# Kernel tuning notes

Hardware: AMD Instinct MI355X
Metric: run time of the kernel (lower is better)

The kernel has to match this reference:

```python
import jax, jax.numpy as jnp
import numpy as np

B, NPG, IN_DIM, H, E = 128, 500, 3, 128, 512000
N = B * NPG
NEG = -1e9  # stands in for -inf masked fill; exp underflows to exactly 0 in fp32
BN_EPS = 1e-5


def setup_inputs() -> dict:
    key = jax.random.key(0)
    ks = jax.random.split(key, 40)
    rn = lambda k, shape: (jax.random.normal(k, shape, jnp.float32) * 0.05)
    x = jax.random.normal(ks[0], (N, IN_DIM), jnp.float32)
    g = jax.random.randint(ks[1], (E,), 0, B)
    src = jax.random.randint(ks[2], (E,), 0, NPG) + g * NPG
    dst = jax.random.randint(ks[3], (E,), 0, NPG) + g * NPG
    edge_index = jnp.stack([src, dst]).astype(jnp.int32)
    batch = (jnp.arange(N) // NPG).astype(jnp.int32)
    feasible_mask = jax.random.uniform(ks[4], (B, NPG, NPG)) < 0.1
    feasible_mask = feasible_mask.at[:, 0, 0].set(True)  # >=1 feasible action/graph
    return dict(
        x=x, edge_index=edge_index, batch=batch, feasible_mask=feasible_mask,
        gin_W1_0=rn(ks[5], (IN_DIM, H)), gin_b1_0=jnp.zeros((H,), jnp.float32),
        gin_g_0=jnp.ones((H,), jnp.float32), gin_be_0=jnp.zeros((H,), jnp.float32),
        gin_W2_0=rn(ks[6], (H, H)), gin_b2_0=jnp.zeros((H,), jnp.float32),
        gin_W1=rn(ks[7], (3, H, H)), gin_b1=jnp.zeros((3, H), jnp.float32),
        gin_g=jnp.ones((3, H), jnp.float32), gin_be=jnp.zeros((3, H), jnp.float32),
        gin_W2=rn(ks[8], (3, H, H)), gin_b2=jnp.zeros((3, H), jnp.float32),
        pol_W1_0=rn(ks[9], (2 * H, H)), pol_b1_0=jnp.zeros((H,), jnp.float32),
        pol_W2_0=rn(ks[10], (H, H)), pol_b2_0=jnp.zeros((H,), jnp.float32),
        pol_W1=rn(ks[11], (2, H, H)), pol_b1=jnp.zeros((2, H), jnp.float32),
        pol_W2=rn(ks[12], (2, H, H)), pol_b2=jnp.zeros((2, H), jnp.float32),
    )


def _gin_conv(h, src, dst, deg, W1, b1, g, be, W2, b2):
    # mean-aggregate neighbors (self loops already in edge list), eps=0
    agg = jax.ops.segment_sum(h[src], dst, num_segments=N) / deg[:, None]
    z = (h + agg) @ W1 + b1
    mu = jnp.mean(z, axis=0)
    var = jnp.var(z, axis=0)  # biased var, as torch BN training mode
    z = (z - mu) * jax.lax.rsqrt(var + BN_EPS) * g + be
    return jax.nn.relu(z) @ W2 + b2


def reference(x, edge_index, batch, feasible_mask,
              gin_W1_0, gin_b1_0, gin_g_0, gin_be_0, gin_W2_0, gin_b2_0,
              gin_W1, gin_b1, gin_g, gin_be, gin_W2, gin_b2,
              pol_W1_0, pol_b1_0, pol_W2_0, pol_b2_0,
              pol_W1, pol_b1, pol_W2, pol_b2):
    # add self loops
    loop = jnp.arange(N, dtype=edge_index.dtype)
    src = jnp.concatenate([edge_index[0], loop])
    dst = jnp.concatenate([edge_index[1], loop])
    deg = jnp.maximum(jax.ops.segment_sum(jnp.ones_like(src, jnp.float32), dst, num_segments=N), 1.0)

    h = _gin_conv(x, src, dst, deg, gin_W1_0, gin_b1_0, gin_g_0, gin_be_0, gin_W2_0, gin_b2_0)
    node_pool = h
    graph_pool = jax.ops.segment_sum(h, batch, num_segments=B) / NPG
    for l in range(3):
        h = _gin_conv(h, src, dst, deg, gin_W1[l], gin_b1[l], gin_g[l], gin_be[l], gin_W2[l], gin_b2[l])
        node_pool = node_pool + h
        graph_pool = graph_pool + jax.ops.segment_sum(h, batch, num_segments=B) / NPG

    # augment node embeds with their graph embed (graphs contiguous, equal size)
    a = jnp.concatenate([node_pool, graph_pool[batch]], axis=-1).reshape(B, NPG, 2 * H)
    a = jnp.tanh(a @ pol_W1_0 + pol_b1_0) @ pol_W2_0 + pol_b2_0
    for l in range(2):
        a = jnp.tanh(a @ pol_W1[l] + pol_b1[l]) @ pol_W2[l] + pol_b2[l]

    scores = jnp.einsum('bnd,bmd->bnm', a, a)                 # [B, n, n]
    scores = jnp.where(feasible_mask, scores, NEG)
    flat = scores.reshape(B, NPG * NPG)
    logp_all = jax.nn.log_softmax(flat, axis=-1)
    actions_id = jax.random.categorical(jax.random.key(42), flat, axis=-1)  # [B]
    log_prob = jnp.take_along_axis(logp_all, actions_id[:, None], axis=1)[:, 0]
    return actions_id, log_prob
```

## Files before the change

### kernel.cpp

```cpp
#include <hip/hip_runtime.h>
#include <float.h>

#define NN 64000
#define BB 128
#define NPGc 500
#define EE 512000

#define SKW(c) ((c) + (((c)>>3)<<2))
#define LW 188

__device__ __forceinline__ unsigned rotl32(unsigned x, unsigned r){ return (x<<r)|(x>>(32u-r)); }

__device__ __forceinline__ unsigned threefry_bits(unsigned idx){
  unsigned x0 = 0u, x1 = idx;
  const unsigned ks0 = 0u, ks1 = 42u, ks2 = 0u ^ 42u ^ 0x1BD11BDAu;
  x0 += ks0; x1 += ks1;
#define RND(r) { x0 += x1; x1 = rotl32(x1, r); x1 ^= x0; }
  RND(13u) RND(15u) RND(26u) RND(6u)   x0 += ks1; x1 += ks2 + 1u;
  RND(17u) RND(29u) RND(16u) RND(24u)  x0 += ks2; x1 += ks0 + 2u;
  RND(13u) RND(15u) RND(26u) RND(6u)   x0 += ks0; x1 += ks1 + 3u;
  RND(17u) RND(29u) RND(16u) RND(24u)  x0 += ks1; x1 += ks2 + 4u;
  RND(13u) RND(15u) RND(26u) RND(6u)   x0 += ks2; x1 += ks0 + 5u;
#undef RND
  return x0 ^ x1;
}

__device__ __forceinline__ float gumbel_of(unsigned idx){
  unsigned bits = threefry_bits(idx);
  float f = __uint_as_float((bits >> 9) | 0x3f800000u) - 1.0f;
  const float TINY = 1.17549435e-38f;
  float u = fmaxf(TINY, f + TINY);
  return -logf(-logf(u));
}

__device__ __forceinline__ float fast_tanh(float x){
  return 1.0f - 2.0f/(__expf(2.0f*x) + 1.0f);
}

__global__ __launch_bounds__(256)
void maskprep_kernel(const unsigned char* __restrict__ mu8src, const int* __restrict__ mi32src,
                     unsigned char* __restrict__ mn8, unsigned char* __restrict__ mt8){
  __shared__ unsigned char tile[64][65];
  const int b = blockIdx.y;
  const int rt = blockIdx.x >> 3, ct = blockIdx.x & 7;
  const int t = threadIdx.x;
  int mybad = (((const unsigned*)mi32src)[t] > 1u) ? 1 : 0;
  int isbool = __syncthreads_or(mybad);
  const int rl = t >> 4;
  const int cq = t & 15;
#pragma unroll
  for (int p=0;p<4;p++){
    int row = rt*64 + p*16 + rl;
    int col = ct*64 + cq*4;
    uchar4 v; v.x=0; v.y=0; v.z=0; v.w=0;
    if (row < NPGc && col < NPGc){
      size_t o = (size_t)b*250000 + (size_t)row*500 + col;
      if (isbool){
        v = *(const uchar4*)(mu8src + o);
      } else {
        int4 w = *(const int4*)(mi32src + o);
        v.x = (unsigned char)(w.x!=0); v.y = (unsigned char)(w.y!=0);
        v.z = (unsigned char)(w.z!=0); v.w = (unsigned char)(w.w!=0);
      }
      *(uchar4*)(mn8 + o) = v;
    }
    int lr = p*16 + rl, lc = cq*4;
    tile[lr][lc+0]=v.x; tile[lr][lc+1]=v.y; tile[lr][lc+2]=v.z; tile[lr][lc+3]=v.w;
  }
  __syncthreads();
#pragma unroll
  for (int p=0;p<4;p++){
    int orow = ct*64 + p*16 + rl;
    int ocol = rt*64 + cq*4;
    if (orow < NPGc && ocol < NPGc){
      uchar4 v;
      v.x = tile[cq*4+0][p*16+rl];
      v.y = tile[cq*4+1][p*16+rl];
      v.z = tile[cq*4+2][p*16+rl];
      v.w = tile[cq*4+3][p*16+rl];
      *(uchar4*)(mt8 + (size_t)b*250000 + (size_t)orow*500 + ocol) = v;
    }
  }
}

__global__ void count_kernel(const int* __restrict__ dst, int* __restrict__ cnt){
  int e = blockIdx.x*256 + threadIdx.x;
  if (e < EE) atomicAdd(&cnt[dst[e]], 1);
}

__global__ void scanA_kernel(const int* __restrict__ cnt, int* __restrict__ bsum){
  __shared__ int red[256];
  int t = threadIdx.x;
  red[t] = cnt[blockIdx.x*256 + t];
  __syncthreads();
  for (int s=128;s>0;s>>=1){
    if (t < s) red[t] += red[t+s];
    __syncthreads();
  }
  if (t == 0) bsum[blockIdx.x] = red[0];
}

__global__ void scanB_kernel(const int* __restrict__ bsum, int* __restrict__ boff){
  __shared__ int red[256];
  int t = threadIdx.x;
  int v = (t < 250) ? bsum[t] : 0;
  red[t] = v;
  __syncthreads();
  for (int d=1; d<256; d<<=1){
    int x = (t >= d) ? red[t-d] : 0;
    __syncthreads();
    red[t] += x;
    __syncthreads();
  }
  if (t < 250) boff[t] = red[t] - v;
  if (t == 249) boff[250] = red[t];
}

__global__ void scanC_kernel(const int* __restrict__ cnt, const int* __restrict__ boff,
                             int* __restrict__ off, int* __restrict__ cur){
  __shared__ int red[256];
  int t = threadIdx.x;
  int n = blockIdx.x*256 + t;
  int v = cnt[n];
  red[t] = v;
  __syncthreads();
  for (int d=1; d<256; d<<=1){
    int x = (t >= d) ? red[t-d] : 0;
    __syncthreads();
    red[t] += x;
    __syncthreads();
  }
  int excl = red[t] - v + boff[blockIdx.x];
  off[n] = excl; cur[n] = excl;
  if (n == NN-1) off[NN] = excl + v;
}

__global__ void fill_kernel(const int* __restrict__ src, const int* __restrict__ dst,
                            int* __restrict__ cur, int* __restrict__ csr){
  int e = blockIdx.x*256 + threadIdx.x;
  if (e < EE){
    int d = dst[e];
    int p = atomicAdd(&cur[d], 1);
    csr[p] = src[e];
  }
}

__global__ __launch_bounds__(256)
void agg128_kernel(const float* __restrict__ h, const int* __restrict__ off,
                   const int* __restrict__ csr, const int* __restrict__ cnt,
                   float* __restrict__ xin){
  const int nb = gridDim.x;
  const int per = nb >> 3;
  int bid = (blockIdx.x % 8)*per + (blockIdx.x >> 3);
  int w = (bid*256 + (int)threadIdx.x) >> 6;
  int lane = threadIdx.x & 63;
  if (w >= NN) return;
  const float* hn = h + (size_t)w*128;
  float a0 = hn[lane], a1 = hn[lane+64];
  float s0 = a0, s1 = a1;
  int e0 = off[w], e1 = off[w+1];
  int e = e0;
  for (; e + 4 <= e1; e += 4){
    int sA = csr[e], sB = csr[e+1], sC = csr[e+2], sD = csr[e+3];
    const float* pA = h + (size_t)sA*128;
    const float* pB = h + (size_t)sB*128;
    const float* pC = h + (size_t)sC*128;
    const float* pD = h + (size_t)sD*128;
    float a0A = pA[lane], a1A = pA[lane+64];
    float a0B = pB[lane], a1B = pB[lane+64];
    float a0C = pC[lane], a1C = pC[lane+64];
    float a0D = pD[lane], a1D = pD[lane+64];
    s0 += a0A; s1 += a1A;
    s0 += a0B; s1 += a1B;
    s0 += a0C; s1 += a1C;
    s0 += a0D; s1 += a1D;
  }
  for (; e < e1; ++e){
    int s = csr[e];
    const float* hs = h + (size_t)s*128;
    s0 += hs[lane]; s1 += hs[lane+64];
  }
  float di = 1.0f/(float)(cnt[w]+1);
  xin[(size_t)w*128 + lane]      = a0 + s0*di;
  xin[(size_t)w*128 + lane + 64] = a1 + s1*di;
}

__global__ __launch_bounds__(256)
void z0_kernel(const float* __restrict__ x, const int* __restrict__ off,
               const int* __restrict__ csr, const int* __restrict__ cnt,
               const float* __restrict__ W, const float* __restrict__ bias,
               float* __restrict__ z, float* __restrict__ stats){
  __shared__ float xr[192];
  __shared__ float ssum[128], ssq[128];
  int t = threadIdx.x;
  int row0 = blockIdx.x*64;
  if (t < 192){
    int nl = t/3, f = t - nl*3;
    int n = row0 + nl;
    float a = x[n*3+f];
    float s = a;
    int e1 = off[n+1];
    for (int e = off[n]; e < e1; ++e) s += x[csr[e]*3 + f];
    float di = 1.0f/(float)(cnt[n]+1);
    xr[t] = a + s*di;
  }
  if (t < 128){ ssum[t]=0.f; ssq[t]=0.f; }
  int f = t & 127, rg = t >> 7;
  float w0 = W[f], w1 = W[128+f], w2 = W[256+f], bb = bias[f];
  __syncthreads();
  float s = 0.f, q = 0.f;
  for (int i=0;i<32;i++){
    int r = rg*32 + i;
    float y = bb + xr[r*3]*w0 + xr[r*3+1]*w1 + xr[r*3+2]*w2;
    z[(size_t)(row0+r)*128 + f] = y;
    s += y; q += y*y;
  }
  atomicAdd(&ssum[f], s); atomicAdd(&ssq[f], q);
  __syncthreads();
  if (t < 128){ atomicAdd(&stats[t], ssum[t]); atomicAdd(&stats[128+t], ssq[t]); }
}

template<int K, bool CATF, bool BNF, bool TANHF, bool STATSF, int POOLM>
__global__ __launch_bounds__(256, 2)
void linear_kernel(const float* X, const float* __restrict__ X2,
                   const float* __restrict__ W, const float* __restrict__ bias,
                   float* Y,
                   const float* __restrict__ statsIn, const float* __restrict__ gam,
                   const float* __restrict__ bet,
                   float* __restrict__ statsOut, float* __restrict__ pool){
  __shared__ __align__(16) float xs[32][LW];
  __shared__ __align__(16) float ws[32][LW];
  __shared__ float ssum[128], ssq[128];
  __shared__ __align__(16) float bnsc_s[128], bnsh_s[128];
  const int t = threadIdx.x;
  const int row0 = blockIdx.x*128;
  const int cg = t & 15, rg = t >> 4;
  const int c0 = cg*8, r0 = rg*8;
  const int skr0 = SKW(r0), skc0 = SKW(c0);
  float acc[8][8];
#pragma unroll
  for (int r=0;r<8;r++)
#pragma unroll
    for (int c=0;c<8;c++) acc[r][c]=0.f;
  if (STATSF && t < 128){ ssum[t]=0.f; ssq[t]=0.f; }
  if (BNF && t < 128){
    float mu  = statsIn[t]     * (1.0f/NN);
    float var = statsIn[128+t] * (1.0f/NN) - mu*mu;
    float rsv = rsqrtf(var + 1e-5f);
    float sc  = gam[t]*rsv;
    bnsc_s[t] = sc;
    bnsh_s[t] = bet[t] - mu*sc;
  }

  for (int kc=0; kc<K; kc+=32){
    __syncthreads();
#pragma unroll
    for (int i=0;i<4;i++){
      int task = t + 256*i;
      int n = task >> 3, k4 = task & 7;
      int gk = kc + k4*4;
      int row = row0 + n;
      float4 v;
      if (CATF){
        if (gk < 128) v = *(const float4*)(X  + (size_t)row*128 + gk);
        else          v = *(const float4*)(X2 + (size_t)(row/NPGc)*128 + (gk-128));
      } else {
        v = *(const float4*)(X + (size_t)row*K + gk);
      }
      if (BNF){
        float4 sc4 = *(const float4*)(bnsc_s + gk);
        float4 sh4 = *(const float4*)(bnsh_s + gk);
        v.x = fmaxf(0.f, v.x*sc4.x + sh4.x);
        v.y = fmaxf(0.f, v.y*sc4.y + sh4.y);
        v.z = fmaxf(0.f, v.z*sc4.z + sh4.z);
        v.w = fmaxf(0.f, v.w*sc4.w + sh4.w);
      }
      int ns = SKW(n);
      xs[k4*4+0][ns] = v.x; xs[k4*4+1][ns] = v.y;
      xs[k4*4+2][ns] = v.z; xs[k4*4+3][ns] = v.w;
    }
#pragma unroll
    for (int i=0;i<4;i++){
      int task = t + 256*i;
      int k = task >> 5, c4 = task & 31;
      float4 v = *(const float4*)(W + (size_t)(kc+k)*128 + c4*4);
      *(float4*)&ws[k][c4*4 + ((c4>>1)<<2)] = v;
    }
    __syncthreads();
#pragma unroll
    for (int k=0;k<32;k++){
      float4 xa = *(const float4*)&xs[k][skr0];
      float4 xb = *(const float4*)&xs[k][skr0+4];
      float4 wa = *(const float4*)&ws[k][skc0];
      float4 wb = *(const float4*)&ws[k][skc0+4];
      float xv[8] = {xa.x,xa.y,xa.z,xa.w,xb.x,xb.y,xb.z,xb.w};
      float wv[8] = {wa.x,wa.y,wa.z,wa.w,wb.x,wb.y,wb.z,wb.w};
#pragma unroll
      for (int r=0;r<8;r++)
#pragma unroll
        for (int c=0;c<8;c++)
          acc[r][c] += xv[r]*wv[c];
    }
  }
  float4 ba = *(const float4*)(bias + c0);
  float4 bb2 = *(const float4*)(bias + c0 + 4);
  float bv[8] = {ba.x,ba.y,ba.z,ba.w,bb2.x,bb2.y,bb2.z,bb2.w};
  float sc8[8], sq8[8];
#pragma unroll
  for (int c=0;c<8;c++){ sc8[c]=0.f; sq8[c]=0.f; }
#pragma unroll
  for (int r=0;r<8;r++){
    int n = row0 + r0 + r;
    float y[8];
#pragma unroll
    for (int c=0;c<8;c++){
      float v = acc[r][c] + bv[c];
      if (TANHF) v = fast_tanh(v);
      y[c] = v;
    }
    float4 y0; y0.x=y[0]; y0.y=y[1]; y0.z=y[2]; y0.w=y[3];
    float4 y1; y1.x=y[4]; y1.y=y[5]; y1.z=y[6]; y1.w=y[7];
    *(float4*)(Y + (size_t)n*128 + c0)     = y0;
    *(float4*)(Y + (size_t)n*128 + c0 + 4) = y1;
    if (POOLM == 1){
      *(float4*)(pool + (size_t)n*128 + c0)     = y0;
      *(float4*)(pool + (size_t)n*128 + c0 + 4) = y1;
    } else if (POOLM == 2){
      float4 p0 = *(const float4*)(pool + (size_t)n*128 + c0);
      float4 p1 = *(const float4*)(pool + (size_t)n*128 + c0 + 4);
      p0.x+=y[0]; p0.y+=y[1]; p0.z+=y[2]; p0.w+=y[3];
      p1.x+=y[4]; p1.y+=y[5]; p1.z+=y[6]; p1.w+=y[7];
      *(float4*)(pool + (size_t)n*128 + c0)     = p0;
      *(float4*)(pool + (size_t)n*128 + c0 + 4) = p1;
    }
    if (STATSF){
#pragma unroll
      for (int c=0;c<8;c++){ sc8[c]+=y[c]; sq8[c]+=y[c]*y[c]; }
    }
  }
  if (STATSF){
#pragma unroll
    for (int c=0;c<8;c++){
      atomicAdd(&ssum[c0+c], sc8[c]);
      atomicAdd(&ssq[c0+c],  sq8[c]);
    }
    __syncthreads();
    if (t < 128){
      atomicAdd(&statsOut[t],     ssum[t]);
      atomicAdd(&statsOut[128+t], ssq[t]);
    }
  }
}

__global__ __launch_bounds__(512)
void gpool_kernel(const float* __restrict__ pool, float* __restrict__ gpool){
  __shared__ float red[4][128];
  int b = blockIdx.x;
  int f = threadIdx.x & 127, part = threadIdx.x >> 7;
  const float* p = pool + (size_t)b*NPGc*128 + f;
  int rbeg = part*125, rend = rbeg + 125;
  float s = 0.f;
  for (int i=rbeg;i<rend;i++) s += p[(size_t)i*128];
  red[part][f] = s;
  __syncthreads();
  if (part == 0){
    float tot = ((red[0][f] + red[1][f]) + red[2][f]) + red[3][f];
    gpool[(size_t)b*128 + f] = tot * (1.0f/NPGc);
  }
}

#define QCAP 1024
#define NPAIR 36

__global__ __launch_bounds__(256)
void scores_tri_kernel(const float* __restrict__ A, const unsigned char* __restrict__ mn8,
                       const unsigned char* __restrict__ mt8, float* __restrict__ partials){
  __shared__ __align__(16) float as[128][68];
  __shared__ __align__(16) float bs[32][68];
  __shared__ float qs[QCAP];
  __shared__ int   qi[QCAP];
  __shared__ int   qcnt;
  float* rm  = qs;
  float* rs_ = qs + 256;
  float* rv  = qs + 512;
  float* rsc = qs + 768;
  int*   ri  = qi;
  const int t = threadIdx.x;
  const int xcd = blockIdx.x & 7;
  const int within = blockIdx.x >> 3;
  const int b = xcd*16 + within/NPAIR;
  int pidx = within % NPAIR, tn = 0;
  while (pidx >= 8 - tn){ pidx -= 8 - tn; tn++; }
  const int tm = tn + pidx;
  const int pair = within % NPAIR;
  const bool diag = (tn == tm);
  const int n0 = tn*64, m0 = tm*64;
  const int cgc = t & 15, rgc = t >> 4;
  const int r0_ = rgc*4, c0 = cgc*4;
  const float* Ab = A + (size_t)b*NPGc*128;
  const unsigned gbase = (unsigned)b*250000u;
  if (t == 0) qcnt = 0;

#pragma unroll
  for (int i=0;i<32;i++){
    int idx = t + 256*i;
    int k = idx & 127, r = idx >> 7;
    int n = n0 + r;
    as[k][r] = (n < NPGc) ? Ab[(size_t)n*128 + k] : 0.f;
  }

  float acc[4][4];
#pragma unroll
  for (int i2=0;i2<4;i2++)
#pragma unroll
    for (int j=0;j<4;j++) acc[i2][j]=0.f;

  for (int kc=0;kc<4;kc++){
    __syncthreads();
#pragma unroll
    for (int i=0;i<8;i++){
      int idx = t + 256*i;
      int kk = idx & 31, c = idx >> 5;
      int m = m0 + c;
      bs[kk][c] = (m < NPGc) ? Ab[(size_t)m*128 + kc*32 + kk] : 0.f;
    }
    __syncthreads();
#pragma unroll
    for (int kk=0;kk<32;kk++){
      float4 av = *(const float4*)&as[kc*32+kk][r0_];
      float4 bv4 = *(const float4*)&bs[kk][c0];
      float a_[4] = {av.x,av.y,av.z,av.w};
      float b_[4] = {bv4.x,bv4.y,bv4.z,bv4.w};
#pragma unroll
      for (int i2=0;i2<4;i2++)
#pragma unroll
        for (int j=0;j<4;j++)
          acc[i2][j] += a_[i2]*b_[j];
    }
  }

  float mrun = -1e30f, srun = 0.f, bval = -FLT_MAX, bsc = 0.f;
  int bidx = 0x7FFFFFFF;
  const int mbase = m0 + c0;
  const bool colok = (mbase < NPGc);
#pragma unroll
  for (int i2=0;i2<4;i2++){
    int n = n0 + r0_ + i2;
    bool rowok = colok && (n < NPGc);
    bool fn[4] = {false,false,false,false};
    bool fm[4] = {false,false,false,false};
    if (rowok){
      size_t moff = (size_t)b*250000 + (size_t)n*500 + (size_t)mbase;
      uchar4 mk = *(const uchar4*)(mn8 + moff);
      fn[0]=mk.x!=0; fn[1]=mk.y!=0; fn[2]=mk.z!=0; fn[3]=mk.w!=0;
      uchar4 tk = *(const uchar4*)(mt8 + moff);
      fm[0]=tk.x!=0; fm[1]=tk.y!=0; fm[2]=tk.z!=0; fm[3]=tk.w!=0;
    }
    float cntj[4], sj[4];
    bool pn[4], pm[4];
#pragma unroll
    for (int j=0;j<4;j++){
      int m = mbase + j;
      bool mok = rowok && (m < NPGc);
      bool keep = mok && (!diag || m >= n);
      bool isde = (n == m);
      float cnt = 0.f; bool a1=false, a2=false;
      if (keep){
        if (isde){ cnt = fn[j] ? 1.f : 0.f; a1 = fn[j]; }
        else { cnt = (fn[j]?1.f:0.f) + (fm[j]?1.f:0.f); a1 = fn[j]; a2 = fm[j]; }
      }
      cntj[j]=cnt; pn[j]=a1; pm[j]=a2;
      sj[j] = (cnt > 0.f) ? acc[i2][j] : -1e30f;
    }
    float tmx = fmaxf(fmaxf(sj[0],sj[1]), fmaxf(sj[2],sj[3]));
    float nm = fmaxf(mrun, tmx);
    float add = 0.f;
#pragma unroll
    for (int j=0;j<4;j++) add += cntj[j]*__expf(sj[j] - nm);
    srun = srun*__expf(mrun - nm) + add;
    mrun = nm;
#pragma unroll
    for (int j=0;j<4;j++){
      int m = mbase + j;
      if (pn[j] || pm[j]){
        float s = acc[i2][j];
#pragma unroll
        for (int d=0;d<2;d++){
          bool doit = d ? pm[j] : pn[j];
          if (doit){
            int lidx = d ? (m*500 + n) : (n*500 + m);
            int slot = atomicAdd(&qcnt, 1);
            if (slot < QCAP){ qs[slot] = s; qi[slot] = lidx; }
            else {
              float g = gumbel_of(gbase + (unsigned)lidx);
              float val = s + g;
              if (val > bval || (val == bval && lidx < bidx)){ bval = val; bidx = lidx; bsc = s; }
            }
          }
        }
      }
    }
  }
  __syncthreads();
  int qn = qcnt; if (qn > QCAP) qn = QCAP;
  for (int i = t; i < qn; i += 256){
    float s = qs[i]; int idx = qi[i];
    float g = gumbel_of(gbase + (unsigned)idx);
    float val = s + g;
    if (val > bval || (val == bval && idx < bidx)){ bval = val; bidx = idx; bsc = s; }
  }
  __syncthreads();
  rm[t]=mrun; rs_[t]=srun; rv[t]=bval; ri[t]=bidx; rsc[t]=bsc;
  __syncthreads();
  for (int offr=128; offr>0; offr>>=1){
    if (t < offr){
      float m1 = rm[t], s1 = rs_[t];
      float m2 = rm[t+offr], s2 = rs_[t+offr];
      float M = fmaxf(m1, m2);
      float S = s1*expf(m1-M) + s2*expf(m2-M);
      rm[t] = M; rs_[t] = S;
      float v2 = rv[t+offr]; int i2_ = ri[t+offr];
      if (v2 > rv[t] || (v2 == rv[t] && i2_ < ri[t])){ rv[t]=v2; ri[t]=i2_; rsc[t]=rsc[t+offr]; }
    }
    __syncthreads();
  }
  if (t == 0){
    float* p = partials + ((size_t)b*NPAIR + pair)*8;
    p[0]=rm[0]; p[1]=rs_[0]; p[2]=rv[0]; p[3]=(float)ri[0]; p[4]=rsc[0];
  }
}

__global__ void finalize_kernel(const float* __restrict__ partials, float* __restrict__ out){
  int b = threadIdx.x;
  float M = -1e30f, S = 0.f, BV = -FLT_MAX, BS = 0.f;
  int BI = 0x7FFFFFFF;
  for (int tp=0; tp<NPAIR; tp++){
    const float* p = partials + ((size_t)b*NPAIR + tp)*8;
    float m = p[0], s = p[1], v = p[2]; int i = (int)p[3]; float sc2 = p[4];
    float nM = fmaxf(M, m);
    S = S*expf(M-nM) + s*expf(m-nM);
    M = nM;
    if (v > BV || (v == BV && i < BI)){ BV = v; BI = i; BS = sc2; }
  }
  out[b]      = (float)BI;
  out[BB + b] = BS - (M + logf(S));
}

extern "C" void kernel_launch(void* const* d_in, const int* in_sizes, int n_in,
                              void* d_out, int out_size, void* d_ws, size_t ws_size,
                              hipStream_t stream){
  const float* x        = (const float*)d_in[0];
  const int*   eidx     = (const int*)d_in[1];
  const void*  maskp    = d_in[3];
  const float* gin_W1_0 = (const float*)d_in[4];
  const float* gin_b1_0 = (const float*)d_in[5];
  const float* gin_g_0  = (const float*)d_in[6];
  const float* gin_be_0 = (const float*)d_in[7];
  const float* gin_W2_0 = (const float*)d_in[8];
  const float* gin_b2_0 = (const float*)d_in[9];
  const float* gin_W1   = (const float*)d_in[10];
  const float* gin_b1   = (const float*)d_in[11];
  const float* gin_g    = (const float*)d_in[12];
  const float* gin_be   = (const float*)d_in[13];
  const float* gin_W2   = (const float*)d_in[14];
  const float* gin_b2   = (const float*)d_in[15];
  const float* pol_W1_0 = (const float*)d_in[16];
  const float* pol_b1_0 = (const float*)d_in[17];
  const float* pol_W2_0 = (const float*)d_in[18];
  const float* pol_b2_0 = (const float*)d_in[19];
  const float* pol_W1   = (const float*)d_in[20];
  const float* pol_b1   = (const float*)d_in[21];
  const float* pol_W2   = (const float*)d_in[22];
  const float* pol_b2   = (const float*)d_in[23];
  float* out = (float*)d_out;

  char* p = (char*)d_ws;
  auto carve = [&](size_t bytes) -> void* {
    void* r = (void*)p; p += (bytes + 255) & ~(size_t)255; return r;
  };
  float* hbuf  = (float*)carve((size_t)NN*128*4);
  float* xin   = (float*)carve((size_t)NN*128*4);
  float* pool  = (float*)carve((size_t)NN*128*4);
  float* gpool = (float*)carve((size_t)BB*128*4);
  float* stats = (float*)carve(4*256*4);
  float* partials = (float*)carve((size_t)BB*NPAIR*8*4);
  int* cnt  = (int*)carve((size_t)NN*4);
  int* off  = (int*)carve((size_t)(NN+1)*4);
  int* cur  = (int*)carve((size_t)NN*4);
  int* csr  = (int*)carve((size_t)EE*4);
  int* bsum = (int*)carve(256*4);
  int* boff = (int*)carve(256*4);
  unsigned char* mn8 = (unsigned char*)carve((size_t)BB*250000);
  unsigned char* mt8 = (unsigned char*)carve((size_t)BB*250000);

  const int* srcp = eidx;
  const int* dstp = eidx + EE;

  {
    dim3 mg(64, BB);
    maskprep_kernel<<<mg, 256, 0, stream>>>((const unsigned char*)maskp, (const int*)maskp,
                                            mn8, mt8);
  }

  hipMemsetAsync(cnt, 0, (size_t)NN*4, stream);
  hipMemsetAsync(stats, 0, 4*256*4, stream);
  count_kernel<<<(EE+255)/256, 256, 0, stream>>>(dstp, cnt);
  scanA_kernel<<<NN/256, 256, 0, stream>>>(cnt, bsum);
  scanB_kernel<<<1, 256, 0, stream>>>(bsum, boff);
  scanC_kernel<<<NN/256, 256, 0, stream>>>(cnt, boff, off, cur);
  fill_kernel<<<(EE+255)/256, 256, 0, stream>>>(srcp, dstp, cur, csr);

  z0_kernel<<<NN/64, 256, 0, stream>>>(x, off, csr, cnt, gin_W1_0, gin_b1_0, xin, stats);
  linear_kernel<128,false,true,false,false,1><<<NN/128, 256, 0, stream>>>(
      xin, nullptr, gin_W2_0, gin_b2_0, hbuf, stats, gin_g_0, gin_be_0, nullptr, pool);

  for (int l=0; l<3; l++){
    float* st = stats + (l+1)*256;
    agg128_kernel<<<NN/4, 256, 0, stream>>>(hbuf, off, csr, cnt, xin);
    linear_kernel<128,false,false,false,true,0><<<NN/128, 256, 0, stream>>>(
        xin, nullptr, gin_W1 + (size_t)l*16384, gin_b1 + l*128, xin,
        nullptr, nullptr, nullptr, st, nullptr);
    linear_kernel<128,false,true,false,false,2><<<NN/128, 256, 0, stream>>>(
        xin, nullptr, gin_W2 + (size_t)l*16384, gin_b2 + l*128, hbuf,
        st, gin_g + l*128, gin_be + l*128, nullptr, pool);
  }

  gpool_kernel<<<BB, 512, 0, stream>>>(pool, gpool);
  linear_kernel<256,true,false,true,false,0><<<NN/128, 256, 0, stream>>>(
      pool, gpool, pol_W1_0, pol_b1_0, hbuf, nullptr, nullptr, nullptr, nullptr, nullptr);
  linear_kernel<128,false,false,false,false,0><<<NN/128, 256, 0, stream>>>(
      hbuf, nullptr, pol_W2_0, pol_b2_0, xin, nullptr, nullptr, nullptr, nullptr, nullptr);
  linear_kernel<128,false,false,true,false,0><<<NN/128, 256, 0, stream>>>(
      xin, nullptr, pol_W1, pol_b1, hbuf, nullptr, nullptr, nullptr, nullptr, nullptr);
  linear_kernel<128,false,false,false,false,0><<<NN/128, 256, 0, stream>>>(
      hbuf, nullptr, pol_W2, pol_b2, xin, nullptr, nullptr, nullptr, nullptr, nullptr);
  linear_kernel<128,false,false,true,false,0><<<NN/128, 256, 0, stream>>>(
      xin, nullptr, pol_W1 + 16384, pol_b1 + 128, hbuf, nullptr, nullptr, nullptr, nullptr, nullptr);
  linear_kernel<128,false,false,false,false,0><<<NN/128, 256, 0, stream>>>(
      hbuf, nullptr, pol_W2 + 16384, pol_b2 + 128, xin, nullptr, nullptr, nullptr, nullptr, nullptr);

  scores_tri_kernel<<<8*16*NPAIR, 256, 0, stream>>>(xin, mn8, mt8, partials);
  finalize_kernel<<<1, BB, 0, stream>>>(partials, out);
}
```

Before: 1.174 ms.

## Enlarge score tiles to 128x128 with 8x8 register blocking

Changes the triangular score kernel from 64x64 tiles (36 pairs per graph) to 128x128 tiles (10 pairs per graph), with 8x8 per-thread accumulators, float4 global loads and skewed shared-memory layout. The candidate queue is now drained after each row of the epilogue so it does not overflow with the larger tile. This is meant to cut redundant A reloads and block count and raise FMA-to-load ratio. In exchange it uses more registers, which can lower occupancy, adds barriers inside the epilogue loop, and wastes more work on the padded tail tile (500 is not a multiple of 128).

```diff
diff --git a/kernel.cpp b/kernel.cpp
--- a/kernel.cpp
+++ b/kernel.cpp
@@ -370,13 +370,13 @@
 }
 
 #define QCAP 1024
-#define NPAIR 36
+#define NPAIR 10
 
 __global__ __launch_bounds__(256)
 void scores_tri_kernel(const float* __restrict__ A, const unsigned char* __restrict__ mn8,
                        const unsigned char* __restrict__ mt8, float* __restrict__ partials){
-  __shared__ __align__(16) float as[128][68];
-  __shared__ __align__(16) float bs[32][68];
+  __shared__ __align__(16) float as[32][LW];
+  __shared__ __align__(16) float bs[32][LW];
   __shared__ float qs[QCAP];
   __shared__ int   qi[QCAP];
   __shared__ int   qcnt;
@@ -389,77 +389,95 @@
   const int xcd = blockIdx.x & 7;
   const int within = blockIdx.x >> 3;
   const int b = xcd*16 + within/NPAIR;
-  int pidx = within % NPAIR, tn = 0;
-  while (pidx >= 8 - tn){ pidx -= 8 - tn; tn++; }
+  const int pair = within % NPAIR;
+  int pidx = pair, tn = 0;
+  while (pidx >= 4 - tn){ pidx -= 4 - tn; tn++; }
   const int tm = tn + pidx;
-  const int pair = within % NPAIR;
   const bool diag = (tn == tm);
-  const int n0 = tn*64, m0 = tm*64;
-  const int cgc = t & 15, rgc = t >> 4;
-  const int r0_ = rgc*4, c0 = cgc*4;
+  const int n0 = tn*128, m0 = tm*128;
+  const int cg = t & 15, rg = t >> 4;
+  const int c0 = cg*8, r0 = rg*8;
+  const int skr0 = SKW(r0), skc0 = SKW(c0);
   const float* Ab = A + (size_t)b*NPGc*128;
   const unsigned gbase = (unsigned)b*250000u;
   if (t == 0) qcnt = 0;
 
-#pragma unroll
-  for (int i=0;i<32;i++){
-    int idx = t + 256*i;
-    int k = idx & 127, r = idx >> 7;
-    int n = n0 + r;
-    as[k][r] = (n < NPGc) ? Ab[(size_t)n*128 + k] : 0.f;
-  }
-
-  float acc[4][4];
-#pragma unroll
-  for (int i2=0;i2<4;i2++)
-#pragma unroll
-    for (int j=0;j<4;j++) acc[i2][j]=0.f;
-
-  for (int kc=0;kc<4;kc++){
-    __syncthreads();
-#pragma unroll
-    for (int i=0;i<8;i++){
-      int idx = t + 256*i;
-      int kk = idx & 31, c = idx >> 5;
-      int m = m0 + c;
-      bs[kk][c] = (m < NPGc) ? Ab[(size_t)m*128 + kc*32 + kk] : 0.f;
-    }
-    __syncthreads();
-#pragma unroll
-    for (int kk=0;kk<32;kk++){
-      float4 av = *(const float4*)&as[kc*32+kk][r0_];
-      float4 bv4 = *(const float4*)&bs[kk][c0];
-      float a_[4] = {av.x,av.y,av.z,av.w};
-      float b_[4] = {bv4.x,bv4.y,bv4.z,bv4.w};
-#pragma unroll
-      for (int i2=0;i2<4;i2++)
-#pragma unroll
-        for (int j=0;j<4;j++)
-          acc[i2][j] += a_[i2]*b_[j];
+  float acc[8][8];
+#pragma unroll
+  for (int r=0;r<8;r++)
+#pragma unroll
+    for (int c=0;c<8;c++) acc[r][c]=0.f;
+
+  for (int kc=0; kc<128; kc+=32){
+    __syncthreads();
+#pragma unroll
+    for (int i=0;i<4;i++){
+      int task = t + 256*i;
+      int n = task >> 3, k4 = task & 7;
+      int gk = kc + k4*4;
+      int gn = n0 + n;
+      float4 v;
+      if (gn < NPGc) v = *(const float4*)(Ab + (size_t)gn*128 + gk);
+      else { v.x=0.f; v.y=0.f; v.z=0.f; v.w=0.f; }
+      int ns = SKW(n);
+      as[k4*4+0][ns] = v.x; as[k4*4+1][ns] = v.y;
+      as[k4*4+2][ns] = v.z; as[k4*4+3][ns] = v.w;
+    }
+#pragma unroll
+    for (int i=0;i<4;i++){
+      int task = t + 256*i;
+      int m = task >> 3, k4 = task & 7;
+      int gk = kc + k4*4;
+      int gm = m0 + m;
+      float4 v;
+      if (gm < NPGc) v = *(const float4*)(Ab + (size_t)gm*128 + gk);
+      else { v.x=0.f; v.y=0.f; v.z=0.f; v.w=0.f; }
+      int ms = SKW(m);
+      bs[k4*4+0][ms] = v.x; bs[k4*4+1][ms] = v.y;
+      bs[k4*4+2][ms] = v.z; bs[k4*4+3][ms] = v.w;
+    }
+    __syncthreads();
+#pragma unroll
+    for (int k=0;k<32;k++){
+      float4 xa = *(const float4*)&as[k][skr0];
+      float4 xb = *(const float4*)&as[k][skr0+4];
+      float4 wa = *(const float4*)&bs[k][skc0];
+      float4 wb = *(const float4*)&bs[k][skc0+4];
+      float xv[8] = {xa.x,xa.y,xa.z,xa.w,xb.x,xb.y,xb.z,xb.w};
+      float wv[8] = {wa.x,wa.y,wa.z,wa.w,wb.x,wb.y,wb.z,wb.w};
+#pragma unroll
+      for (int r=0;r<8;r++)
+#pragma unroll
+        for (int c=0;c<8;c++)
+          acc[r][c] += xv[r]*wv[c];
     }
   }
 
   float mrun = -1e30f, srun = 0.f, bval = -FLT_MAX, bsc = 0.f;
   int bidx = 0x7FFFFFFF;
   const int mbase = m0 + c0;
-  const bool colok = (mbase < NPGc);
-#pragma unroll
-  for (int i2=0;i2<4;i2++){
-    int n = n0 + r0_ + i2;
-    bool rowok = colok && (n < NPGc);
-    bool fn[4] = {false,false,false,false};
-    bool fm[4] = {false,false,false,false};
+  __syncthreads();
+#pragma unroll
+  for (int r=0;r<8;r++){
+    int n = n0 + r0 + r;
+    bool rowok = (n < NPGc) && (mbase < NPGc);
+    bool fn[8] = {false,false,false,false,false,false,false,false};
+    bool fm[8] = {false,false,false,false,false,false,false,false};
     if (rowok){
       size_t moff = (size_t)b*250000 + (size_t)n*500 + (size_t)mbase;
-      uchar4 mk = *(const uchar4*)(mn8 + moff);
-      fn[0]=mk.x!=0; fn[1]=mk.y!=0; fn[2]=mk.z!=0; fn[3]=mk.w!=0;
-      uchar4 tk = *(const uchar4*)(mt8 + moff);
-      fm[0]=tk.x!=0; fm[1]=tk.y!=0; fm[2]=tk.z!=0; fm[3]=tk.w!=0;
-    }
-    float cntj[4], sj[4];
-    bool pn[4], pm[4];
-#pragma unroll
-    for (int j=0;j<4;j++){
+      uchar4 k0 = *(const uchar4*)(mn8 + moff);
+      uchar4 k1 = *(const uchar4*)(mn8 + moff + 4);
+      fn[0]=k0.x!=0; fn[1]=k0.y!=0; fn[2]=k0.z!=0; fn[3]=k0.w!=0;
+      fn[4]=k1.x!=0; fn[5]=k1.y!=0; fn[6]=k1.z!=0; fn[7]=k1.w!=0;
+      uchar4 t0 = *(const uchar4*)(mt8 + moff);
+      uchar4 t1 = *(const uchar4*)(mt8 + moff + 4);
+      fm[0]=t0.x!=0; fm[1]=t0.y!=0; fm[2]=t0.z!=0; fm[3]=t0.w!=0;
+      fm[4]=t1.x!=0; fm[5]=t1.y!=0; fm[6]=t1.z!=0; fm[7]=t1.w!=0;
+    }
+    float cntj[8], sj[8];
+    bool pn[8], pm[8];
+#pragma unroll
+    for (int j=0;j<8;j++){
       int m = mbase + j;
       bool mok = rowok && (m < NPGc);
       bool keep = mok && (!diag || m >= n);
@@ -470,20 +488,22 @@
         else { cnt = (fn[j]?1.f:0.f) + (fm[j]?1.f:0.f); a1 = fn[j]; a2 = fm[j]; }
       }
       cntj[j]=cnt; pn[j]=a1; pm[j]=a2;
-      sj[j] = (cnt > 0.f) ? acc[i2][j] : -1e30f;
-    }
-    float tmx = fmaxf(fmaxf(sj[0],sj[1]), fmaxf(sj[2],sj[3]));
+      sj[j] = (cnt > 0.f) ? acc[r][j] : -1e30f;
+    }
+    float tmx = sj[0];
+#pragma unroll
+    for (int j=1;j<8;j++) tmx = fmaxf(tmx, sj[j]);
     float nm = fmaxf(mrun, tmx);
     float add = 0.f;
 #pragma unroll
-    for (int j=0;j<4;j++) add += cntj[j]*__expf(sj[j] - nm);
+    for (int j=0;j<8;j++) add += cntj[j]*__expf(sj[j] - nm);
     srun = srun*__expf(mrun - nm) + add;
     mrun = nm;
 #pragma unroll
-    for (int j=0;j<4;j++){
+    for (int j=0;j<8;j++){
       int m = mbase + j;
       if (pn[j] || pm[j]){
-        float s = acc[i2][j];
+        float s = acc[r][j];
 #pragma unroll
         for (int d=0;d<2;d++){
           bool doit = d ? pm[j] : pn[j];
@@ -500,16 +520,18 @@
         }
       }
     }
-  }
-  __syncthreads();
-  int qn = qcnt; if (qn > QCAP) qn = QCAP;
-  for (int i = t; i < qn; i += 256){
-    float s = qs[i]; int idx = qi[i];
-    float g = gumbel_of(gbase + (unsigned)idx);
-    float val = s + g;
-    if (val > bval || (val == bval && idx < bidx)){ bval = val; bidx = idx; bsc = s; }
-  }
-  __syncthreads();
+    __syncthreads();
+    int qn = qcnt; if (qn > QCAP) qn = QCAP;
+    for (int i = t; i < qn; i += 256){
+      float s = qs[i]; int idx = qi[i];
+      float g = gumbel_of(gbase + (unsigned)idx);
+      float val = s + g;
+      if (val > bval || (val == bval && idx < bidx)){ bval = val; bidx = idx; bsc = s; }
+    }
+    __syncthreads();
+    if (t == 0) qcnt = 0;
+    __syncthreads();
+  }
   rm[t]=mrun; rs_[t]=srun; rv[t]=bval; ri[t]=bidx; rsc[t]=bsc;
   __syncthreads();
   for (int offr=128; offr>0; offr>>=1){
```

New measurement: 1.326 ms. 12.9% more time.
